# Kernel optimization log

Measured on AMD Instinct MI355X. Metric: run time of the kernel, lower is better.

Reference implementation:

```python
import jax, jax.numpy as jnp
import numpy as np

N_HEADS = 16
HEAD_DIM = 64
WINDOW = 128
GLOBAL = 64


def setup_inputs() -> dict:
    key = jax.random.key(0)
    ks = jax.random.split(key, 5)
    B, T, D = 2, 8192, 1024
    s = 0.02
    return {
        "x": jax.random.normal(ks[0], (B, T, D), dtype=jnp.float32),
        "Wq": jax.random.normal(ks[1], (D, D), dtype=jnp.float32) * s,
        "Wk": jax.random.normal(ks[2], (D, D), dtype=jnp.float32) * s,
        "Wv": jax.random.normal(ks[3], (D, D), dtype=jnp.float32) * s,
        "Wo": jax.random.normal(ks[4], (D, D), dtype=jnp.float32) * s,
    }


def reference(x, Wq, Wk, Wv, Wo):
    B, T, D = x.shape
    h, hd, w = N_HEADS, HEAD_DIM, WINDOW
    g = min(GLOBAL, T)
    nw = T // w  # T chosen as a multiple of window_size
    scale = hd ** -0.5

    def proj(W):
        # nn.Linear: y = x @ W.T ; then (B,T,h,hd) -> (B,h,T,hd)
        return (x @ W.T).reshape(B, T, h, hd).transpose(0, 2, 1, 3)

    q = proj(Wq)
    k = proj(Wk)
    v = proj(Wv)

    # Chunk into non-overlapping local windows: (B,h,nw,w,hd)
    qw = q.reshape(B, h, nw, w, hd)
    kw = k.reshape(B, h, nw, w, hd)
    vw = v.reshape(B, h, nw, w, hd)
    kg = k[:, :, :g, :]  # global prefix keys (B,h,g,hd)
    vg = v[:, :, :g, :]

    # Scores against [global ++ local] keys (faithful: global prefix is
    # concatenated for every window, including windows that overlap it).
    s_g = jnp.einsum("bhnqd,bhgd->bhnqg", qw, kg) * scale  # (B,h,nw,w,g)
    s_l = jnp.einsum("bhnqd,bhnkd->bhnqk", qw, kw) * scale  # (B,h,nw,w,w)
    attn = jax.nn.softmax(jnp.concatenate([s_g, s_l], axis=-1), axis=-1)

    out = (
        jnp.einsum("bhnqg,bhgd->bhnqd", attn[..., :g], vg)
        + jnp.einsum("bhnqk,bhnkd->bhnqd", attn[..., g:], vw)
    )
    out = out.reshape(B, h, T, hd).transpose(0, 2, 1, 3).reshape(B, T, D)
    return out @ Wo.T
```

## Files before the change

kernel.cpp:

```cpp
#include <hip/hip_runtime.h>

typedef unsigned short u16;
typedef __attribute__((ext_vector_type(8))) short short8;
typedef __attribute__((ext_vector_type(4))) float f32x4;
typedef __attribute__((ext_vector_type(4))) float floatx4;
typedef __attribute__((ext_vector_type(4))) unsigned short ushort4v;
typedef __attribute__((ext_vector_type(8))) unsigned short ushort8v;

#define MFMA(a, b, c)   __builtin_amdgcn_mfma_f32_16x16x32_bf16(a, b, c, 0, 0, 0)

__device__ __forceinline__ u16 f2bf(float f) {
    unsigned u = __float_as_uint(f);
    u += 0x7fffu + ((u >> 16) & 1u);
    return (u16)(u >> 16);
}

__device__ __forceinline__ void async16(const void* g, void* l) {
    __builtin_amdgcn_global_load_lds(
        (const __attribute__((address_space(1))) void*)g,
        (__attribute__((address_space(3))) void*)l, 16, 0, 0);
}

#define SYNC(n) do {                                             \
    asm volatile("s_waitcnt vmcnt(" #n ")" ::: "memory");        \
    __builtin_amdgcn_s_barrier();                                \
    asm volatile("" ::: "memory");                               \
    __builtin_amdgcn_sched_barrier(0);                           \
} while (0)

__global__ void cvt_all(const float* __restrict__ x,
                        const float* __restrict__ w0, const float* __restrict__ w1,
                        const float* __restrict__ w2, const float* __restrict__ w3,
                        u16* __restrict__ d, int nx4, int nw4) {
    int total = nx4 + 4 * nw4;
    int i = blockIdx.x * blockDim.x + threadIdx.x;
    int stride = gridDim.x * blockDim.x;
    for (; i < total; i += stride) {
        floatx4 v;
        if (i < nx4) {
            v = ((const floatx4*)x)[i];
        } else {
            int t = i - nx4;
            int w = t >> 18;
            int j = t & (nw4 - 1);
            const float* s = w == 0 ? w0 : (w == 1 ? w1 : (w == 2 ? w2 : w3));
            v = ((const floatx4*)s)[j];
        }
        ushort4v o;
        o[0] = f2bf(v[0]); o[1] = f2bf(v[1]); o[2] = f2bf(v[2]); o[3] = f2bf(v[3]);
        ((ushort4v*)d)[i] = o;
    }
}

template <bool BF16_OUT>
__global__ __launch_bounds__(512, 2) void gemm_nt(
    const u16* __restrict__ A, const u16* __restrict__ B0,
    const u16* __restrict__ B1, const u16* __restrict__ B2,
    void* __restrict__ Cv, int M, int N, int K)
{
    __shared__ u16 As[2][16384];
    __shared__ u16 Bs[2][16384];
    const int tid = threadIdx.x;
    const int wave = tid >> 6, lane = tid & 63;
    const int tl = lane & 15, quad = lane >> 4, xr = lane & 7;
    const int wm = wave >> 2, wn = wave & 3;
    const int m0 = blockIdx.x * 256, n0 = blockIdx.y * 256;
    const u16* Bm = blockIdx.z == 0 ? B0 : (blockIdx.z == 1 ? B1 : B2);
    const size_t coff = (size_t)blockIdx.z * M * N;

    f32x4 acc[8][4];
#pragma unroll
    for (int i = 0; i < 8; i++)
#pragma unroll
        for (int j = 0; j < 4; j++) acc[i][j] = (f32x4)(0.0f);

    const int rw = lane >> 3, sl = lane & 7;
    const int g = sl ^ rw;
    const u16* a_srcb = A  + (size_t)(m0 + wave * 8 + rw) * K + g * 8;
    const u16* b_srcb = Bm + (size_t)(n0 + (wave >> 2) * 64 + (wave & 3) * 8 + rw) * K + g * 8;
    u16* asd = &As[0][0] + wave * 512;
    u16* bsd = &Bs[0][0] + (wave >> 2) * 4096 + (wave & 3) * 512;

#define STG_A(t, h, p) do {                                                              \
    async16(a_srcb + (size_t)((h) * 64) * K + (size_t)(t) * 64,                          \
            asd + (p) * 16384 + (h) * 4096);                                             \
    async16(a_srcb + (size_t)((h) * 64 + 128) * K + (size_t)(t) * 64,                    \
            asd + (p) * 16384 + (h) * 4096 + 8192);                                      \
} while (0)
#define STG_B(t, h, p) do {                                                              \
    async16(b_srcb + (size_t)((h) * 32) * K + (size_t)(t) * 64,                          \
            bsd + (p) * 16384 + (h) * 2048);                                             \
    async16(b_srcb + (size_t)((h) * 32 + 128) * K + (size_t)(t) * 64,                    \
            bsd + (p) * 16384 + (h) * 2048 + 8192);                                      \
} while (0)

    const int NT = K >> 6;
    const u16* Ab0 = &As[0][0] + (wm * 128 + tl) * 64;
    const u16* Bb0 = &Bs[0][0] + (wn * 64 + tl) * 64;
    const int s0 = (quad ^ xr) * 8;

    short8 afA[4][2], afB[4][2], bfA[2][2], bfB[2][2];

    STG_A(0, 0, 0); STG_B(0, 0, 0); STG_A(0, 1, 0); STG_B(0, 1, 0);

    for (int t = 0; t < NT; ++t) {
        const int p = t & 1, pq = p ^ 1;
        const bool pf = (t + 1) < NT;
        const u16* Ab = Ab0 + p * 16384;
        const u16* Bb = Bb0 + p * 16384;

        SYNC(4);
#pragma unroll
        for (int i = 0; i < 4; i++) {
            afA[i][0] = *(const short8*)(Ab + i * 1024 + s0);
            afA[i][1] = *(const short8*)(Ab + i * 1024 + (s0 ^ 32));
        }
#pragma unroll
        for (int j = 0; j < 2; j++) {
            bfA[j][0] = *(const short8*)(Bb + j * 1024 + s0);
            bfA[j][1] = *(const short8*)(Bb + j * 1024 + (s0 ^ 32));
        }
        if (pf) STG_A(t + 1, 0, pq);
        __builtin_amdgcn_s_setprio(1);
#pragma unroll
        for (int kh = 0; kh < 2; kh++)
#pragma unroll
            for (int i = 0; i < 4; i++)
#pragma unroll
                for (int j = 0; j < 2; j++)
                    acc[i][j] = MFMA(afA[i][kh], bfA[j][kh], acc[i][j]);
        __builtin_amdgcn_s_setprio(0);

        if (pf) { SYNC(4); } else { SYNC(2); }
#pragma unroll
        for (int i = 0; i < 4; i++) {
            afB[i][0] = *(const short8*)(Ab + (4 + i) * 1024 + s0);
            afB[i][1] = *(const short8*)(Ab + (4 + i) * 1024 + (s0 ^ 32));
        }
        if (pf) STG_B(t + 1, 0, pq);
        __builtin_amdgcn_s_setprio(1);
#pragma unroll
        for (int kh = 0; kh < 2; kh++)
#pragma unroll
            for (int i = 0; i < 4; i++)
#pragma unroll
                for (int j = 0; j < 2; j++)
                    acc[4 + i][j] = MFMA(afB[i][kh], bfA[j][kh], acc[4 + i][j]);
        __builtin_amdgcn_s_setprio(0);

        if (pf) { SYNC(4); } else { SYNC(0); }
#pragma unroll
        for (int j = 0; j < 2; j++) {
            bfB[j][0] = *(const short8*)(Bb + (2 + j) * 1024 + s0);
            bfB[j][1] = *(const short8*)(Bb + (2 + j) * 1024 + (s0 ^ 32));
        }
        if (pf) STG_A(t + 1, 1, pq);
        __builtin_amdgcn_s_setprio(1);
#pragma unroll
        for (int kh = 0; kh < 2; kh++)
#pragma unroll
            for (int i = 0; i < 4; i++)
#pragma unroll
                for (int j = 0; j < 2; j++)
                    acc[4 + i][2 + j] = MFMA(afB[i][kh], bfB[j][kh], acc[4 + i][2 + j]);
        __builtin_amdgcn_s_setprio(0);

        if (pf) STG_B(t + 1, 1, pq);
        __builtin_amdgcn_s_setprio(1);
#pragma unroll
        for (int kh = 0; kh < 2; kh++)
#pragma unroll
            for (int i = 0; i < 4; i++)
#pragma unroll
                for (int j = 0; j < 2; j++)
                    acc[i][2 + j] = MFMA(afA[i][kh], bfB[j][kh], acc[i][2 + j]);
        __builtin_amdgcn_s_setprio(0);
    }
#undef STG_A
#undef STG_B

#pragma unroll
    for (int mf = 0; mf < 8; mf++)
#pragma unroll
        for (int nf = 0; nf < 4; nf++)
#pragma unroll
            for (int r = 0; r < 4; r++) {
                int row = m0 + wm * 128 + mf * 16 + quad * 4 + r;
                int col = n0 + wn * 64 + nf * 16 + tl;
                if constexpr (BF16_OUT)
                    ((u16*)Cv)[coff + (size_t)row * N + col] = f2bf(acc[mf][nf][r]);
                else
                    ((float*)Cv)[coff + (size_t)row * N + col] = acc[mf][nf][r];
            }
}

__global__ __launch_bounds__(256) void attn_win(
    const u16* __restrict__ qkv, u16* __restrict__ outb)
{
    constexpr int T = 8192, D = 1024, HD = 64, G = 64, WIN = 128;
    constexpr int MTOT = 2 * T;
    __shared__ u16 Vt[64 * 200];
    __shared__ u16 KP[12800];

    const int blk = blockIdx.x;
    const int half = blk & 1;
    const int nwin = (blk >> 1) & 63;
    const int h = (blk >> 7) & 15;
    const int b = blk >> 11;
    const int tid = threadIdx.x;
    const int wave = tid >> 6, lane = tid & 63;
    const int quad = lane >> 4, tl = lane & 15;
    const int win0 = nwin * WIN;
    const int q0 = win0 + half * 64;
    const size_t brow = (size_t)b * T;
    const u16* qb = qkv;
    const u16* kb = qkv + (size_t)MTOT * D;
    const u16* vb = qkv + (size_t)2 * MTOT * D;

#pragma unroll
    for (int i = 0; i < 6; i++) {
        int ch = i * 256 + tid;
        int row = ch >> 3, c = ch & 7;
        int tok = row < G ? row : win0 + (row - G);
        async16(vb + (brow + tok) * D + h * HD + c * 8,
                (u16*)KP + (i * 256 + wave * 64) * 8);
    }

    short8 bq[2];
    {
        int tok = q0 + wave * 16 + tl;
        const u16* qrow = qb + (brow + tok) * D + h * HD;
        bq[0] = *(const short8*)(qrow + quad * 8);
        bq[1] = *(const short8*)(qrow + 32 + quad * 8);
    }

    __syncthreads();

    {
        const int d = tid & 63;
#pragma unroll
        for (int i = 0; i < 6; i++) {
            int c = i * 4 + wave;
            ushort8v v;
#pragma unroll
            for (int j = 0; j < 8; j++) v[j] = KP[(c * 8 + j) * 64 + d];
            *(ushort8v*)&Vt[d * 200 + c * 8] = v;
        }
    }

    __syncthreads();

#pragma unroll
    for (int i = 0; i < 6; i++) {
        int ch = i * 256 + tid;
        int row = ch >> 3, slot = ch & 7;
        int g = slot ^ (row & 7);
        int tok = row < G ? row : win0 + (row - G);
        async16(kb + (brow + tok) * D + h * HD + g * 8,
                (u16*)KP + (i * 256 + wave * 64) * 8);
    }

    __syncthreads();

    f32x4 s[12];
#pragma unroll
    for (int kt = 0; kt < 12; kt++) s[kt] = (f32x4)(0.0f);
#pragma unroll
    for (int kt = 0; kt < 12; kt++) {
        int row = kt * 16 + tl;
        int s0 = quad ^ (tl & 7);
        int s1 = (4 + quad) ^ (tl & 7);
        short8 a0 = *(const short8*)&KP[row * 64 + s0 * 8];
        short8 a1 = *(const short8*)&KP[row * 64 + s1 * 8];
        s[kt] = MFMA(a0, bq[0], s[kt]);
        s[kt] = MFMA(a1, bq[1], s[kt]);
    }

    const float c1 = 0.125f * 1.4426950408889634f;
    float mx = -1e30f;
#pragma unroll
    for (int kt = 0; kt < 12; kt++)
#pragma unroll
        for (int r = 0; r < 4; r++) mx = fmaxf(mx, s[kt][r]);
    mx = fmaxf(mx, __shfl_xor(mx, 16, 64));
    mx = fmaxf(mx, __shfl_xor(mx, 32, 64));
    float sum = 0.f;
#pragma unroll
    for (int kt = 0; kt < 12; kt++)
#pragma unroll
        for (int r = 0; r < 4; r++) {
            float e = exp2f((s[kt][r] - mx) * c1);
            s[kt][r] = e;
            sum += e;
        }
    sum += __shfl_xor(sum, 16, 64);
    sum += __shfl_xor(sum, 32, 64);
    float inv = 1.f / sum;

    __syncthreads();

    u16* Pl = (u16*)KP;
    {
        int lq = wave * 16 + tl;
#pragma unroll
        for (int kt = 0; kt < 12; kt++) {
            ushort4v p;
#pragma unroll
            for (int r = 0; r < 4; r++) p[r] = f2bf(s[kt][r] * inv);
            *(ushort4v*)&Pl[lq * 200 + kt * 16 + quad * 4] = p;
        }
    }
    __syncthreads();

    f32x4 o[4];
#pragma unroll
    for (int dt = 0; dt < 4; dt++) o[dt] = (f32x4)(0.0f);
#pragma unroll
    for (int ks = 0; ks < 6; ks++) {
        short8 pa = *(const short8*)&Pl[(wave * 16 + tl) * 200 + ks * 32 + quad * 8];
#pragma unroll
        for (int dt = 0; dt < 4; dt++) {
            short8 vv = *(const short8*)&Vt[(dt * 16 + tl) * 200 + ks * 32 + quad * 8];
            o[dt] = MFMA(pa, vv, o[dt]);
        }
    }

#pragma unroll
    for (int dt = 0; dt < 4; dt++)
#pragma unroll
        for (int r = 0; r < 4; r++) {
            int qq = q0 + wave * 16 + quad * 4 + r;
            int dim = dt * 16 + tl;
            outb[(brow + qq) * D + h * HD + dim] = f2bf(o[dt][r]);
        }
}

extern "C" void kernel_launch(void* const* d_in, const int* in_sizes, int n_in,
                              void* d_out, int out_size, void* d_ws, size_t ws_size,
                              hipStream_t stream)
{
    const float* x  = (const float*)d_in[0];
    const float* Wq = (const float*)d_in[1];
    const float* Wk = (const float*)d_in[2];
    const float* Wv = (const float*)d_in[3];
    const float* Wo = (const float*)d_in[4];

    const int M = 16384, D = 1024;
    u16* xb  = (u16*)d_ws;
    u16* wqb = xb  + (size_t)M * D;
    u16* wob = wqb + (size_t)3 * D * D;
    u16* qkv = wob + (size_t)D * D;
    u16* att = qkv + (size_t)3 * M * D;

    cvt_all<<<2560, 256, 0, stream>>>(x, Wq, Wk, Wv, Wo, xb,
                                      M * D / 4, D * D / 4);

    gemm_nt<true ><<<dim3(M / 256, D / 256, 3), 512, 0, stream>>>(
        xb, wqb, wqb + (size_t)D * D, wqb + (size_t)2 * D * D, qkv, M, D, D);
    attn_win<<<dim3(4096), 256, 0, stream>>>(qkv, att);
    gemm_nt<false><<<dim3(M / 256, D / 256, 1), 512, 0, stream>>>(
        att, wob, wob, wob, d_out, M, D, D);
}
```

Baseline: 305.8 us.

## Deepen GEMM prefetch pipeline and merge attention halves into one 512-thread block

The GEMM main loop now prefetches stage halves two steps ahead into the freed buffer halves, with fixed vmcnt waits and extra barriers in place of the per-phase conditional syncs. Each stage clamps its prefetch index so the pipeline needs no branches. The attention kernel processes a whole 128-query window per 512-thread block, loads K and V concurrently into separate LDS buffers, and stores P in a swizzled layout reusing those buffers. This halves redundant K/V loads per window and overlaps more memory traffic, at the cost of more barriers and higher LDS use per block.

```diff
diff --git a/kernel.cpp b/kernel.cpp
--- a/kernel.cpp
+++ b/kernel.cpp
@@ -21,10 +21,10 @@
         (__attribute__((address_space(3))) void*)l, 16, 0, 0);
 }
 
-#define SYNC(n) do {                                             \
-    asm volatile("s_waitcnt vmcnt(" #n ")" ::: "memory");        \
+#define PSYNC do {                                               \
+    asm volatile("s_waitcnt vmcnt(6)" ::: "memory");             \
     __builtin_amdgcn_s_barrier();                                \
-    asm volatile("" ::: "memory");                               \
+    asm volatile("s_waitcnt lgkmcnt(0)" ::: "memory");           \
     __builtin_amdgcn_sched_barrier(0);                           \
 } while (0)
 
@@ -77,9 +77,9 @@
     const int rw = lane >> 3, sl = lane & 7;
     const int g = sl ^ rw;
     const u16* a_srcb = A  + (size_t)(m0 + wave * 8 + rw) * K + g * 8;
-    const u16* b_srcb = Bm + (size_t)(n0 + (wave >> 2) * 64 + (wave & 3) * 8 + rw) * K + g * 8;
+    const u16* b_srcb = Bm + (size_t)(n0 + wm * 64 + wn * 8 + rw) * K + g * 8;
     u16* asd = &As[0][0] + wave * 512;
-    u16* bsd = &Bs[0][0] + (wave >> 2) * 4096 + (wave & 3) * 512;
+    u16* bsd = &Bs[0][0] + wm * 4096 + wn * 512;
 
 #define STG_A(t, h, p) do {                                                              \
     async16(a_srcb + (size_t)((h) * 64) * K + (size_t)(t) * 64,                          \
@@ -102,14 +102,19 @@
     short8 afA[4][2], afB[4][2], bfA[2][2], bfB[2][2];
 
     STG_A(0, 0, 0); STG_B(0, 0, 0); STG_A(0, 1, 0); STG_B(0, 1, 0);
+    STG_A(1, 0, 1); STG_B(1, 0, 1);
+    asm volatile("s_waitcnt vmcnt(8)" ::: "memory");
+    __builtin_amdgcn_s_barrier();
+    __builtin_amdgcn_sched_barrier(0);
 
     for (int t = 0; t < NT; ++t) {
-        const int p = t & 1, pq = p ^ 1;
-        const bool pf = (t + 1) < NT;
+        const int p = t & 1;
+        const int t1 = (t + 1 < NT) ? t + 1 : NT - 1;
+        const int t2 = (t + 2 < NT) ? t + 2 : NT - 1;
+        const int b1 = (t + 1) & 1, b2 = t & 1;
         const u16* Ab = Ab0 + p * 16384;
         const u16* Bb = Bb0 + p * 16384;
 
-        SYNC(4);
 #pragma unroll
         for (int i = 0; i < 4; i++) {
             afA[i][0] = *(const short8*)(Ab + i * 1024 + s0);
@@ -120,7 +125,8 @@
             bfA[j][0] = *(const short8*)(Bb + j * 1024 + s0);
             bfA[j][1] = *(const short8*)(Bb + j * 1024 + (s0 ^ 32));
         }
-        if (pf) STG_A(t + 1, 0, pq);
+        STG_A(t1, 1, b1);
+        PSYNC;
         __builtin_amdgcn_s_setprio(1);
 #pragma unroll
         for (int kh = 0; kh < 2; kh++)
@@ -130,14 +136,15 @@
                 for (int j = 0; j < 2; j++)
                     acc[i][j] = MFMA(afA[i][kh], bfA[j][kh], acc[i][j]);
         __builtin_amdgcn_s_setprio(0);
-
-        if (pf) { SYNC(4); } else { SYNC(2); }
+        __builtin_amdgcn_s_barrier();
+
 #pragma unroll
         for (int i = 0; i < 4; i++) {
             afB[i][0] = *(const short8*)(Ab + (4 + i) * 1024 + s0);
             afB[i][1] = *(const short8*)(Ab + (4 + i) * 1024 + (s0 ^ 32));
         }
-        if (pf) STG_B(t + 1, 0, pq);
+        STG_B(t1, 1, b1);
+        PSYNC;
         __builtin_amdgcn_s_setprio(1);
 #pragma unroll
         for (int kh = 0; kh < 2; kh++)
@@ -147,14 +154,15 @@
                 for (int j = 0; j < 2; j++)
                     acc[4 + i][j] = MFMA(afB[i][kh], bfA[j][kh], acc[4 + i][j]);
         __builtin_amdgcn_s_setprio(0);
-
-        if (pf) { SYNC(4); } else { SYNC(0); }
+        __builtin_amdgcn_s_barrier();
+
 #pragma unroll
         for (int j = 0; j < 2; j++) {
             bfB[j][0] = *(const short8*)(Bb + (2 + j) * 1024 + s0);
             bfB[j][1] = *(const short8*)(Bb + (2 + j) * 1024 + (s0 ^ 32));
         }
-        if (pf) STG_A(t + 1, 1, pq);
+        STG_A(t2, 0, b2);
+        PSYNC;
         __builtin_amdgcn_s_setprio(1);
 #pragma unroll
         for (int kh = 0; kh < 2; kh++)
@@ -164,8 +172,10 @@
                 for (int j = 0; j < 2; j++)
                     acc[4 + i][2 + j] = MFMA(afB[i][kh], bfB[j][kh], acc[4 + i][2 + j]);
         __builtin_amdgcn_s_setprio(0);
-
-        if (pf) STG_B(t + 1, 1, pq);
+        __builtin_amdgcn_s_barrier();
+
+        STG_B(t2, 0, b2);
+        PSYNC;
         __builtin_amdgcn_s_setprio(1);
 #pragma unroll
         for (int kh = 0; kh < 2; kh++)
@@ -175,9 +185,11 @@
                 for (int j = 0; j < 2; j++)
                     acc[i][2 + j] = MFMA(afA[i][kh], bfB[j][kh], acc[i][2 + j]);
         __builtin_amdgcn_s_setprio(0);
+        __builtin_amdgcn_s_barrier();
     }
 #undef STG_A
 #undef STG_B
+    asm volatile("s_waitcnt vmcnt(0)" ::: "memory");
 
 #pragma unroll
     for (int mf = 0; mf < 8; mf++)
@@ -194,73 +206,74 @@
             }
 }
 
-__global__ __launch_bounds__(256) void attn_win(
+__global__ __launch_bounds__(512) void attn_win(
     const u16* __restrict__ qkv, u16* __restrict__ outb)
 {
     constexpr int T = 8192, D = 1024, HD = 64, G = 64, WIN = 128;
     constexpr int MTOT = 2 * T;
+    __shared__ u16 Vs[192 * 64];
+    __shared__ u16 Ks[192 * 64];
     __shared__ u16 Vt[64 * 200];
-    __shared__ u16 KP[12800];
 
     const int blk = blockIdx.x;
-    const int half = blk & 1;
-    const int nwin = (blk >> 1) & 63;
-    const int h = (blk >> 7) & 15;
-    const int b = blk >> 11;
+    const int nwin = blk & 63;
+    const int h = (blk >> 6) & 15;
+    const int b = blk >> 10;
     const int tid = threadIdx.x;
     const int wave = tid >> 6, lane = tid & 63;
     const int quad = lane >> 4, tl = lane & 15;
     const int win0 = nwin * WIN;
-    const int q0 = win0 + half * 64;
     const size_t brow = (size_t)b * T;
     const u16* qb = qkv;
     const u16* kb = qkv + (size_t)MTOT * D;
     const u16* vb = qkv + (size_t)2 * MTOT * D;
 
-#pragma unroll
-    for (int i = 0; i < 6; i++) {
-        int ch = i * 256 + tid;
+    short8 bq[2];
+    {
+        int tok = win0 + wave * 16 + tl;
+        const u16* qrow = qb + (brow + tok) * D + h * HD;
+        bq[0] = *(const short8*)(qrow + quad * 8);
+        bq[1] = *(const short8*)(qrow + 32 + quad * 8);
+    }
+    __builtin_amdgcn_sched_barrier(0);
+
+#pragma unroll
+    for (int i = 0; i < 3; i++) {
+        int ch = i * 512 + tid;
         int row = ch >> 3, c = ch & 7;
         int tok = row < G ? row : win0 + (row - G);
         async16(vb + (brow + tok) * D + h * HD + c * 8,
-                (u16*)KP + (i * 256 + wave * 64) * 8);
-    }
-
-    short8 bq[2];
+                Vs + (i * 512 + wave * 64) * 8);
+    }
+#pragma unroll
+    for (int i = 0; i < 3; i++) {
+        int ch = i * 512 + tid;
+        int row = ch >> 3, slot = ch & 7;
+        int gg = slot ^ (row & 7);
+        int tok = row < G ? row : win0 + (row - G);
+        async16(kb + (brow + tok) * D + h * HD + gg * 8,
+                Ks + (i * 512 + wave * 64) * 8);
+    }
+
+    asm volatile("s_waitcnt vmcnt(3)" ::: "memory");
+    __builtin_amdgcn_s_barrier();
+    __builtin_amdgcn_sched_barrier(0);
+
     {
-        int tok = q0 + wave * 16 + tl;
-        const u16* qrow = qb + (brow + tok) * D + h * HD;
-        bq[0] = *(const short8*)(qrow + quad * 8);
-        bq[1] = *(const short8*)(qrow + 32 + quad * 8);
-    }
-
-    __syncthreads();
-
-    {
-        const int d = tid & 63;
-#pragma unroll
-        for (int i = 0; i < 6; i++) {
-            int c = i * 4 + wave;
+        const int d = lane;
+#pragma unroll
+        for (int i = 0; i < 3; i++) {
+            int c = wave * 3 + i;
             ushort8v v;
 #pragma unroll
-            for (int j = 0; j < 8; j++) v[j] = KP[(c * 8 + j) * 64 + d];
+            for (int j = 0; j < 8; j++) v[j] = Vs[(c * 8 + j) * 64 + d];
             *(ushort8v*)&Vt[d * 200 + c * 8] = v;
         }
     }
 
-    __syncthreads();
-
-#pragma unroll
-    for (int i = 0; i < 6; i++) {
-        int ch = i * 256 + tid;
-        int row = ch >> 3, slot = ch & 7;
-        int g = slot ^ (row & 7);
-        int tok = row < G ? row : win0 + (row - G);
-        async16(kb + (brow + tok) * D + h * HD + g * 8,
-                (u16*)KP + (i * 256 + wave * 64) * 8);
-    }
-
-    __syncthreads();
+    asm volatile("s_waitcnt vmcnt(0) lgkmcnt(0)" ::: "memory");
+    __builtin_amdgcn_s_barrier();
+    __builtin_amdgcn_sched_barrier(0);
 
     f32x4 s[12];
 #pragma unroll
@@ -268,10 +281,10 @@
 #pragma unroll
     for (int kt = 0; kt < 12; kt++) {
         int row = kt * 16 + tl;
-        int s0 = quad ^ (tl & 7);
-        int s1 = (4 + quad) ^ (tl & 7);
-        short8 a0 = *(const short8*)&KP[row * 64 + s0 * 8];
-        short8 a1 = *(const short8*)&KP[row * 64 + s1 * 8];
+        int sa = quad ^ (tl & 7);
+        int sb = (4 + quad) ^ (tl & 7);
+        short8 a0 = *(const short8*)&Ks[row * 64 + sa * 8];
+        short8 a1 = *(const short8*)&Ks[row * 64 + sb * 8];
         s[kt] = MFMA(a0, bq[0], s[kt]);
         s[kt] = MFMA(a1, bq[1], s[kt]);
     }
@@ -299,16 +312,14 @@
 
     __syncthreads();
 
-    u16* Pl = (u16*)KP;
-    {
-        int lq = wave * 16 + tl;
-#pragma unroll
-        for (int kt = 0; kt < 12; kt++) {
-            ushort4v p;
-#pragma unroll
-            for (int r = 0; r < 4; r++) p[r] = f2bf(s[kt][r] * inv);
-            *(ushort4v*)&Pl[lq * 200 + kt * 16 + quad * 4] = p;
-        }
+    const int lq = wave * 16 + tl;
+    u16* Pr = (lq < 64) ? (Vs + lq * 192) : (Ks + (lq - 64) * 192);
+#pragma unroll
+    for (int kt = 0; kt < 12; kt++) {
+        ushort4v pk;
+#pragma unroll
+        for (int r = 0; r < 4; r++) pk[r] = f2bf(s[kt][r] * inv);
+        *(ushort4v*)&Pr[((((kt * 2) + (quad >> 1)) ^ (lq & 7)) << 3) + ((quad & 1) << 2)] = pk;
     }
     __syncthreads();
 
@@ -317,7 +328,7 @@
     for (int dt = 0; dt < 4; dt++) o[dt] = (f32x4)(0.0f);
 #pragma unroll
     for (int ks = 0; ks < 6; ks++) {
-        short8 pa = *(const short8*)&Pl[(wave * 16 + tl) * 200 + ks * 32 + quad * 8];
+        short8 pa = *(const short8*)&Pr[(((ks * 4) + quad) ^ (lq & 7)) << 3];
 #pragma unroll
         for (int dt = 0; dt < 4; dt++) {
             short8 vv = *(const short8*)&Vt[(dt * 16 + tl) * 200 + ks * 32 + quad * 8];
@@ -329,7 +340,7 @@
     for (int dt = 0; dt < 4; dt++)
 #pragma unroll
         for (int r = 0; r < 4; r++) {
-            int qq = q0 + wave * 16 + quad * 4 + r;
+            int qq = win0 + wave * 16 + quad * 4 + r;
             int dim = dt * 16 + tl;
             outb[(brow + qq) * D + h * HD + dim] = f2bf(o[dt][r]);
         }
@@ -357,7 +368,7 @@
 
     gemm_nt<true ><<<dim3(M / 256, D / 256, 3), 512, 0, stream>>>(
         xb, wqb, wqb + (size_t)D * D, wqb + (size_t)2 * D * D, qkv, M, D, D);
-    attn_win<<<dim3(4096), 256, 0, stream>>>(qkv, att);
+    attn_win<<<dim3(2048), 512, 0, stream>>>(qkv, att);
     gemm_nt<false><<<dim3(M / 256, D / 256, 1), 512, 0, stream>>>(
         att, wob, wob, wob, d_out, M, D, D);
 }
```

After: 320.9 us. 4.9% more time.
